# Kernel tuning notes

Measured on AMD Instinct MI355X. Metric: run time of the kernel, lower is better.

The kernel has to match this reference:

```python
import jax, jax.numpy as jnp
import numpy as np
import math

D_MODEL = 1024
D_STATE = 64
BATCH = 16
LENGTH = 4096


def _hippo_legs(n_dim: int) -> np.ndarray:
    """HiPPO-LegS matrix, scaled by 0.5 as in the torch module."""
    n = np.arange(n_dim)[:, None].astype(np.float32)
    k = np.arange(n_dim)[None, :].astype(np.float32)
    a = np.where(n > k, -np.sqrt(2.0 * n + 1.0) * np.sqrt(2.0 * k + 1.0), 0.0)
    a = a + np.diag(-(np.arange(n_dim, dtype=np.float32) + 1.0))
    return (a * 0.5).astype(np.float32)


def setup_inputs() -> dict:
    key = jax.random.key(0)
    k_u, k_B, k_C, k_dt = jax.random.split(key, 4)
    u = jax.random.normal(k_u, (BATCH, LENGTH, D_MODEL), dtype=jnp.float32)
    A = jnp.asarray(_hippo_legs(D_STATE))
    B = jax.random.normal(k_B, (D_STATE, D_MODEL), dtype=jnp.float32) * 0.01
    C = jax.random.normal(k_C, (D_MODEL, D_STATE), dtype=jnp.float32) * 0.01
    D = jnp.ones((D_MODEL,), dtype=jnp.float32)
    log_dt = (jax.random.uniform(k_dt, (D_MODEL,), dtype=jnp.float32)
              * (math.log(0.1) - math.log(0.001)) + math.log(0.001))
    return {"u": u, "A": A, "B": B, "C": C, "D": D, "log_dt": log_dt}


def reference(u, A, B, C, D, log_dt):
    # u: (B, L, d_model)
    d_state = A.shape[0]
    dt_mean = jnp.exp(log_dt).mean()
    a_bar = jnp.eye(d_state, dtype=u.dtype) + dt_mean * A  # (N, N)
    # Precompute input projection for every timestep: (L, B, N)
    bu = jnp.einsum('bld,nd->lbn', u, dt_mean * B)

    def step(x, bu_t):
        # x: (B, N); x_{t} = x_{t-1} @ a_bar.T + (u_t @ b_bar.T)
        x = x @ a_bar.T + bu_t
        return x, x

    x0 = jnp.zeros((u.shape[0], d_state), dtype=u.dtype)
    _, xs = jax.lax.scan(step, x0, bu)  # xs: (L, B, N)
    y = jnp.einsum('lbn,dn->bld', xs, C) + u * D  # (B, L, d_model)
    return y
```

## Files before the change

### kernel.cpp

```cpp
#include <hip/hip_runtime.h>


#define DM   1024
#define DS   64
#define NB   16
#define LL   4096
#define LC   64
#define NCH  (LL / LC)
#define MTOT (NB * LL)
#define NTASK (NB * NCH)

#define WS_ABAR 64
#define WS_APOW (WS_ABAR + 4096)
#define WS_TMP  (WS_APOW + 4096)
#define WS_E    (WS_TMP + 4096)
#define WS_S    (WS_E + NTASK * DS)
#define WS_BHI  143424
#define WS_CHI  (WS_BHI + 32768)
#define WS_XS   (WS_CHI + 32768)
#define WS_BU   (WS_XS + 2097152)

typedef __attribute__((ext_vector_type(4))) float f32x4;
typedef __attribute__((ext_vector_type(8))) short bf16x8;
typedef __attribute__((ext_vector_type(8))) unsigned short ushort8;

__device__ inline unsigned short bf16_rne(float f) {
    unsigned u = __builtin_bit_cast(unsigned, f);
    u += 0x7FFFu + ((u >> 16) & 1u);
    return (unsigned short)(u >> 16);
}

__global__ __launch_bounds__(256) void k_prep(const float* __restrict__ A,
                                              const float* __restrict__ log_dt,
                                              float* __restrict__ ws) {
    __shared__ float red[256];
    int tid = threadIdx.x;
    float s = 0.f;
    for (int i = tid; i < DM; i += 256) s += expf(log_dt[i]);
    red[tid] = s;
    __syncthreads();
    for (int off = 128; off > 0; off >>= 1) {
        if (tid < off) red[tid] += red[tid + off];
        __syncthreads();
    }
    float dt = red[0] * (1.f / (float)DM);
    if (tid == 0) ws[0] = dt;
    for (int idx = tid; idx < 4096; idx += 256) {
        int n = idx >> 6, m = idx & 63;
        ws[WS_ABAR + idx] = dt * A[idx] + ((n == m) ? 1.f : 0.f);
    }
}

__global__ __launch_bounds__(256) void k_cvt(const float* __restrict__ Bm,
                                             const float* __restrict__ C,
                                             float* __restrict__ ws) {
    int bid = blockIdx.x;
    int isC = bid >> 6;
    const float* src = isC ? C : Bm;
    unsigned short* dst = (unsigned short*)(ws + (isC ? WS_CHI : WS_BHI));
    float scale = isC ? 1.f : ws[0];
    int i = ((bid & 63) * 256 + threadIdx.x) * 4;
    float4 v = *reinterpret_cast<const float4*>(&src[i]);
    ushort4 h;
    h.x = bf16_rne(v.x * scale);
    h.y = bf16_rne(v.y * scale);
    h.z = bf16_rne(v.z * scale);
    h.w = bf16_rne(v.w * scale);
    *reinterpret_cast<ushort4*>(&dst[i]) = h;
}

__global__ __launch_bounds__(256) void k_matsq(const float* __restrict__ src,
                                               float* __restrict__ dst) {
    __shared__ float s[64][65];
    int tid = threadIdx.x;
#pragma unroll
    for (int rep = 0; rep < 16; ++rep) {
        int idx = rep * 256 + tid;
        s[idx >> 6][idx & 63] = src[idx];
    }
    __syncthreads();
    int n = (blockIdx.x << 2) + (tid >> 6);
    int m = tid & 63;
    float a0 = 0.f, a1 = 0.f, a2 = 0.f, a3 = 0.f;
#pragma unroll
    for (int k = 0; k < 64; k += 4) {
        a0 = fmaf(s[n][k + 0], s[k + 0][m], a0);
        a1 = fmaf(s[n][k + 1], s[k + 1][m], a1);
        a2 = fmaf(s[n][k + 2], s[k + 2][m], a2);
        a3 = fmaf(s[n][k + 3], s[k + 3][m], a3);
    }
    dst[(n << 6) + m] = (a0 + a1) + (a2 + a3);
}

__global__ __launch_bounds__(256, 4) void k_gemm1(const float* __restrict__ u,
                                                  const float* __restrict__ ws,
                                                  float* __restrict__ bu) {
    __shared__ short a_t[64][72];
    __shared__ short b_t[64][72];
    const unsigned short* bhig = (const unsigned short*)(ws + WS_BHI);
    int tid = threadIdx.x;
    int m0 = blockIdx.x * 64;
    int wid = tid >> 6, lane = tid & 63;
    int lr = lane & 15, lg = lane >> 4;
    int sr = tid >> 3, sc8 = (tid & 7) << 3;
    int bn = tid >> 3, bk8 = (tid & 7) << 3;

    f32x4 acc[4];
#pragma unroll
    for (int j = 0; j < 4; ++j) acc[j] = (f32x4)(0.f);

    float4 ra[2][2];
    ushort8 rb[2];
#pragma unroll
    for (int i = 0; i < 2; ++i) {
        ra[i][0] = *reinterpret_cast<const float4*>(&u[(size_t)(m0 + sr + 32 * i) * DM + sc8]);
        ra[i][1] = *reinterpret_cast<const float4*>(&u[(size_t)(m0 + sr + 32 * i) * DM + sc8 + 4]);
    }
#pragma unroll
    for (int j = 0; j < 2; ++j)
        rb[j] = *reinterpret_cast<const ushort8*>(&bhig[(size_t)(bn + 32 * j) * DM + bk8]);

    for (int kt = 0; kt < 16; ++kt) {
#pragma unroll
        for (int i = 0; i < 2; ++i) {
            ushort8 h;
            h[0] = bf16_rne(ra[i][0].x); h[1] = bf16_rne(ra[i][0].y);
            h[2] = bf16_rne(ra[i][0].z); h[3] = bf16_rne(ra[i][0].w);
            h[4] = bf16_rne(ra[i][1].x); h[5] = bf16_rne(ra[i][1].y);
            h[6] = bf16_rne(ra[i][1].z); h[7] = bf16_rne(ra[i][1].w);
            *reinterpret_cast<ushort8*>(&a_t[sr + 32 * i][sc8]) = h;
        }
#pragma unroll
        for (int j = 0; j < 2; ++j)
            *reinterpret_cast<ushort8*>(&b_t[bn + 32 * j][bk8]) = rb[j];
        __syncthreads();
        if (kt + 1 < 16) {
            int k0n = (kt + 1) * 64;
#pragma unroll
            for (int i = 0; i < 2; ++i) {
                ra[i][0] = *reinterpret_cast<const float4*>(&u[(size_t)(m0 + sr + 32 * i) * DM + k0n + sc8]);
                ra[i][1] = *reinterpret_cast<const float4*>(&u[(size_t)(m0 + sr + 32 * i) * DM + k0n + sc8 + 4]);
            }
#pragma unroll
            for (int j = 0; j < 2; ++j)
                rb[j] = *reinterpret_cast<const ushort8*>(&bhig[(size_t)(bn + 32 * j) * DM + k0n + bk8]);
        }
#pragma unroll
        for (int kf = 0; kf < 2; ++kf) {
            int kb = kf * 32 + lg * 8;
            bf16x8 af = *reinterpret_cast<bf16x8*>(&a_t[wid * 16 + lr][kb]);
#pragma unroll
            for (int nf = 0; nf < 4; ++nf) {
                bf16x8 bf_ = *reinterpret_cast<bf16x8*>(&b_t[nf * 16 + lr][kb]);
                acc[nf] = __builtin_amdgcn_mfma_f32_16x16x32_bf16(af, bf_, acc[nf], 0, 0, 0);
            }
        }
        __syncthreads();
    }
#pragma unroll
    for (int nf = 0; nf < 4; ++nf)
#pragma unroll
        for (int q = 0; q < 4; ++q) {
            size_t row = (size_t)(m0 + wid * 16 + lg * 4 + q);
            bu[row * DS + nf * 16 + lr] = acc[nf][q];
        }
}

template <int PASS>
__global__ __launch_bounds__(256) void k_scan(float* __restrict__ ws) {
    const float* Abar = ws + WS_ABAR;
    float* bu = ws + WS_BU;
    unsigned short* xs = (unsigned short*)(ws + WS_XS);
    int tid = threadIdx.x;
    int w = tid >> 6, lane = tid & 63;
    int t0 = blockIdx.x * 4 + w;
    int t1 = t0 + 512;
    __shared__ float xbuf[4][2][64];

    float a_row[64];
#pragma unroll
    for (int mg = 0; mg < 16; ++mg) {
        float4 v = *reinterpret_cast<const float4*>(&Abar[lane * 64 + mg * 4]);
        a_row[mg * 4 + 0] = v.x; a_row[mg * 4 + 1] = v.y;
        a_row[mg * 4 + 2] = v.z; a_row[mg * 4 + 3] = v.w;
    }
    float x0, x1;
    if (PASS == 0) { x0 = 0.f; x1 = 0.f; }
    else {
        x0 = ws[WS_S + (size_t)t0 * DS + lane];
        x1 = ws[WS_S + (size_t)t1 * DS + lane];
    }
    size_t r0 = (size_t)(t0 >> 6) * LL + (size_t)(t0 & 63) * LC;
    size_t r1 = (size_t)(t1 >> 6) * LL + (size_t)(t1 & 63) * LC;
    float* bub0 = bu + r0 * DS;
    float* bub1 = bu + r1 * DS;
    unsigned short* xp0 = xs + r0 * DS;
    unsigned short* xp1 = xs + r1 * DS;
    float v0 = bub0[lane], v1 = bub1[lane];
    for (int t = 0; t < LC; ++t) {
        float n0 = 0.f, n1 = 0.f;
        if (t + 1 < LC) {
            n0 = bub0[(t + 1) * DS + lane];
            n1 = bub1[(t + 1) * DS + lane];
        }
        xbuf[w][0][lane] = x0;
        xbuf[w][1][lane] = x1;
        asm volatile("" ::: "memory");
        float p0[4], p1[4];
#pragma unroll
        for (int g = 0; g < 4; ++g) {
            float acc0 = (g == 0) ? v0 : 0.f;
            float acc1 = (g == 0) ? v1 : 0.f;
#pragma unroll
            for (int q = 0; q < 4; ++q) {
                float4 m0v = *reinterpret_cast<float4*>(&xbuf[w][0][g * 16 + q * 4]);
                float4 m1v = *reinterpret_cast<float4*>(&xbuf[w][1][g * 16 + q * 4]);
                float c0 = a_row[g * 16 + q * 4 + 0], c1 = a_row[g * 16 + q * 4 + 1];
                float c2 = a_row[g * 16 + q * 4 + 2], c3 = a_row[g * 16 + q * 4 + 3];
                acc0 = fmaf(c0, m0v.x, acc0); acc1 = fmaf(c0, m1v.x, acc1);
                acc0 = fmaf(c1, m0v.y, acc0); acc1 = fmaf(c1, m1v.y, acc1);
                acc0 = fmaf(c2, m0v.z, acc0); acc1 = fmaf(c2, m1v.z, acc1);
                acc0 = fmaf(c3, m0v.w, acc0); acc1 = fmaf(c3, m1v.w, acc1);
            }
            p0[g] = acc0; p1[g] = acc1;
        }
        asm volatile("" ::: "memory");
        x0 = (p0[0] + p0[1]) + (p0[2] + p0[3]);
        x1 = (p1[0] + p1[1]) + (p1[2] + p1[3]);
        if (PASS == 1) {
            xp0[t * DS + lane] = bf16_rne(x0);
            xp1[t * DS + lane] = bf16_rne(x1);
        }
        v0 = n0; v1 = n1;
    }
    if (PASS == 0) {
        ws[WS_E + (size_t)t0 * DS + lane] = x0;
        ws[WS_E + (size_t)t1 * DS + lane] = x1;
    }
}

__global__ __launch_bounds__(64) void k_combine(float* __restrict__ ws) {
    const float* Apow = ws + WS_APOW;
    int b = blockIdx.x;
    int lane = threadIdx.x;
    __shared__ float xbuf[64];
    __shared__ float e_lds[NCH][64];
    const float* Eb = ws + WS_E + (size_t)b * NCH * DS;
#pragma unroll
    for (int r = 0; r < 16; ++r) {
        int idx = r * 64 + lane;
        int jj = idx >> 4, c4 = (idx & 15) << 2;
        *reinterpret_cast<float4*>(&e_lds[jj][c4]) =
            *reinterpret_cast<const float4*>(&Eb[jj * DS + c4]);
    }
    float p_row[64];
#pragma unroll
    for (int mg = 0; mg < 16; ++mg) {
        float4 v = *reinterpret_cast<const float4*>(&Apow[lane * 64 + mg * 4]);
        p_row[mg * 4 + 0] = v.x; p_row[mg * 4 + 1] = v.y;
        p_row[mg * 4 + 2] = v.z; p_row[mg * 4 + 3] = v.w;
    }
    __syncthreads();
    float x = 0.f;
    for (int jj = 0; jj < NCH; ++jj) {
        size_t task = (size_t)b * NCH + jj;
        ws[WS_S + task * DS + lane] = x;
        float e = e_lds[jj][lane];
        xbuf[lane] = x;
        asm volatile("" ::: "memory");
        float part[4];
#pragma unroll
        for (int g = 0; g < 4; ++g) {
            float acc = (g == 0) ? e : 0.f;
#pragma unroll
            for (int q = 0; q < 4; ++q) {
                float4 xm = *reinterpret_cast<float4*>(&xbuf[g * 16 + q * 4]);
                acc = fmaf(p_row[g * 16 + q * 4 + 0], xm.x, acc);
                acc = fmaf(p_row[g * 16 + q * 4 + 1], xm.y, acc);
                acc = fmaf(p_row[g * 16 + q * 4 + 2], xm.z, acc);
                acc = fmaf(p_row[g * 16 + q * 4 + 3], xm.w, acc);
            }
            part[g] = acc;
        }
        asm volatile("" ::: "memory");
        x = (part[0] + part[1]) + (part[2] + part[3]);
    }
}

__global__ __launch_bounds__(256, 4) void k_gemm2(const float* __restrict__ u,
                                                  const float* __restrict__ Dv,
                                                  const float* __restrict__ ws,
                                                  float* __restrict__ y) {
    __shared__ __align__(16) char smem[2 * 128 * 72 * 2];
    short (*a_t)[72] = (short(*)[72])(smem);
    short (*c_t)[72] = (short(*)[72])(smem + 18432);
    float (*out_lds)[132] = (float(*)[132])(smem);

    const unsigned short* xsb = (const unsigned short*)(ws + WS_XS);
    const unsigned short* chig = (const unsigned short*)(ws + WS_CHI);
    int tid = threadIdx.x;
    int m0 = blockIdx.x * 128;
    int d0 = blockIdx.y * 128;
    int wid = tid >> 6, lane = tid & 63;
    int lr = lane & 15, lg = lane >> 4;

#pragma unroll
    for (int rep = 0; rep < 4; ++rep) {
        int idx = rep * 256 + tid;
        int r = idx >> 3, k8 = (idx & 7) << 3;
        *reinterpret_cast<ushort8*>(&a_t[r][k8]) =
            *reinterpret_cast<const ushort8*>(&xsb[(size_t)(m0 + r) * DS + k8]);
    }
#pragma unroll
    for (int rep = 0; rep < 4; ++rep) {
        int idx = rep * 256 + tid;
        int dl = idx >> 3, n8 = (idx & 7) << 3;
        *reinterpret_cast<ushort8*>(&c_t[dl][n8]) =
            *reinterpret_cast<const ushort8*>(&chig[(size_t)(d0 + dl) * DS + n8]);
    }
    __syncthreads();

    f32x4 acc[2][8];
#pragma unroll
    for (int i = 0; i < 2; ++i)
#pragma unroll
        for (int j = 0; j < 8; ++j) acc[i][j] = (f32x4)(0.f);

#pragma unroll
    for (int kf = 0; kf < 2; ++kf) {
        int kb = kf * 32 + lg * 8;
        bf16x8 ah0 = *reinterpret_cast<bf16x8*>(&a_t[wid * 32 + lr][kb]);
        bf16x8 ah1 = *reinterpret_cast<bf16x8*>(&a_t[wid * 32 + 16 + lr][kb]);
#pragma unroll
        for (int nf = 0; nf < 8; ++nf) {
            bf16x8 cb = *reinterpret_cast<bf16x8*>(&c_t[nf * 16 + lr][kb]);
            acc[0][nf] = __builtin_amdgcn_mfma_f32_16x16x32_bf16(ah0, cb, acc[0][nf], 0, 0, 0);
            acc[1][nf] = __builtin_amdgcn_mfma_f32_16x16x32_bf16(ah1, cb, acc[1][nf], 0, 0, 0);
        }
    }
    __syncthreads();

#pragma unroll
    for (int h = 0; h < 2; ++h) {
        if ((wid >> 1) == h) {
            int rbase = (wid & 1) * 32;
#pragma unroll
            for (int mf = 0; mf < 2; ++mf)
#pragma unroll
                for (int nf = 0; nf < 8; ++nf)
#pragma unroll
                    for (int q = 0; q < 4; ++q)
                        out_lds[rbase + mf * 16 + lg * 4 + q][nf * 16 + lr] = acc[mf][nf][q];
        }
        __syncthreads();
#pragma unroll
        for (int rep = 0; rep < 8; ++rep) {
            int idx = rep * 256 + tid;
            int r = idx >> 5, c4 = (idx & 31) << 2;
            float4 a = *reinterpret_cast<float4*>(&out_lds[r][c4]);
            size_t row = (size_t)(m0 + h * 64 + r);
            int c = d0 + c4;
            float4 uv = *reinterpret_cast<const float4*>(&u[row * DM + c]);
            float4 dv = *reinterpret_cast<const float4*>(&Dv[c]);
            float4 o;
            o.x = a.x + uv.x * dv.x;
            o.y = a.y + uv.y * dv.y;
            o.z = a.z + uv.z * dv.z;
            o.w = a.w + uv.w * dv.w;
            *reinterpret_cast<float4*>(&y[row * DM + c]) = o;
        }
        __syncthreads();
    }
}

extern "C" void kernel_launch(void* const* d_in, const int* in_sizes, int n_in,
                              void* d_out, int out_size, void* d_ws, size_t ws_size,
                              hipStream_t stream) {
    (void)in_sizes; (void)n_in; (void)out_size; (void)ws_size;
    const float* u      = (const float*)d_in[0];
    const float* A      = (const float*)d_in[1];
    const float* Bm     = (const float*)d_in[2];
    const float* C      = (const float*)d_in[3];
    const float* Dv     = (const float*)d_in[4];
    const float* log_dt = (const float*)d_in[5];
    float* y  = (float*)d_out;
    float* ws = (float*)d_ws;
    float* bu = ws + WS_BU;

    k_prep<<<dim3(1), dim3(256), 0, stream>>>(A, log_dt, ws);
    k_cvt<<<dim3(128), dim3(256), 0, stream>>>(Bm, C, ws);
    k_matsq<<<dim3(16), dim3(256), 0, stream>>>(ws + WS_ABAR, ws + WS_TMP);
    k_matsq<<<dim3(16), dim3(256), 0, stream>>>(ws + WS_TMP,  ws + WS_APOW);
    k_matsq<<<dim3(16), dim3(256), 0, stream>>>(ws + WS_APOW, ws + WS_TMP);
    k_matsq<<<dim3(16), dim3(256), 0, stream>>>(ws + WS_TMP,  ws + WS_APOW);
    k_matsq<<<dim3(16), dim3(256), 0, stream>>>(ws + WS_APOW, ws + WS_TMP);
    k_matsq<<<dim3(16), dim3(256), 0, stream>>>(ws + WS_TMP,  ws + WS_APOW);

    k_gemm1<<<dim3(MTOT / 64), dim3(256), 0, stream>>>(u, ws, bu);
    k_scan<0><<<dim3(NTASK / 8), dim3(256), 0, stream>>>(ws);
    k_combine<<<dim3(NB), dim3(64), 0, stream>>>(ws);
    k_scan<1><<<dim3(NTASK / 8), dim3(256), 0, stream>>>(ws);
    k_gemm2<<<dim3(MTOT / 128, DM / 128), dim3(256), 0, stream>>>(u, Dv, ws, y);
}
```

Baseline: 349.6 us.

## Scan two timesteps per iteration using A^2 to halve serial dependency chain

The chunked scan now advances the state two steps at a time via x_{t+2} = A^2 x_t + (A b_t + b_{t+1}), keeping A^2 rows in registers, so the dependent matvec chain per chunk is halved. Each wave handles one chunk instead of two, and twice as many blocks are launched. The input-projection matvec is off the critical path, and pass 1 recomputes odd states separately. In exchange the per-step FLOPs and register pressure (two 64-float rows) go up. A trailing __syncthreads in gemm2 is also dropped on the last half-iteration.

```diff
diff --git a/kernel.cpp b/kernel.cpp
--- a/kernel.cpp
+++ b/kernel.cpp
@@ -11,11 +11,12 @@
 #define NTASK (NB * NCH)
 
 #define WS_ABAR 64
-#define WS_APOW (WS_ABAR + 4096)
-#define WS_TMP  (WS_APOW + 4096)
-#define WS_E    (WS_TMP + 4096)
+#define WS_A2   4160
+#define WS_APOW 8256
+#define WS_TMP  12352
+#define WS_E    16448
 #define WS_S    (WS_E + NTASK * DS)
-#define WS_BHI  143424
+#define WS_BHI  (WS_S + NTASK * DS)
 #define WS_CHI  (WS_BHI + 32768)
 #define WS_XS   (WS_CHI + 32768)
 #define WS_BU   (WS_XS + 2097152)
@@ -169,74 +170,94 @@
 template <int PASS>
 __global__ __launch_bounds__(256) void k_scan(float* __restrict__ ws) {
     const float* Abar = ws + WS_ABAR;
+    const float* A2m  = ws + WS_A2;
     float* bu = ws + WS_BU;
     unsigned short* xs = (unsigned short*)(ws + WS_XS);
     int tid = threadIdx.x;
     int w = tid >> 6, lane = tid & 63;
-    int t0 = blockIdx.x * 4 + w;
-    int t1 = t0 + 512;
-    __shared__ float xbuf[4][2][64];
-
-    float a_row[64];
+    int task = blockIdx.x * 4 + w;
+    __shared__ float xbuf[4][64];
+    __shared__ float bbuf[4][2][64];
+
+    float a_row[64], a2_row[64];
 #pragma unroll
     for (int mg = 0; mg < 16; ++mg) {
         float4 v = *reinterpret_cast<const float4*>(&Abar[lane * 64 + mg * 4]);
         a_row[mg * 4 + 0] = v.x; a_row[mg * 4 + 1] = v.y;
         a_row[mg * 4 + 2] = v.z; a_row[mg * 4 + 3] = v.w;
-    }
-    float x0, x1;
-    if (PASS == 0) { x0 = 0.f; x1 = 0.f; }
-    else {
-        x0 = ws[WS_S + (size_t)t0 * DS + lane];
-        x1 = ws[WS_S + (size_t)t1 * DS + lane];
-    }
-    size_t r0 = (size_t)(t0 >> 6) * LL + (size_t)(t0 & 63) * LC;
-    size_t r1 = (size_t)(t1 >> 6) * LL + (size_t)(t1 & 63) * LC;
-    float* bub0 = bu + r0 * DS;
-    float* bub1 = bu + r1 * DS;
-    unsigned short* xp0 = xs + r0 * DS;
-    unsigned short* xp1 = xs + r1 * DS;
-    float v0 = bub0[lane], v1 = bub1[lane];
-    for (int t = 0; t < LC; ++t) {
-        float n0 = 0.f, n1 = 0.f;
-        if (t + 1 < LC) {
-            n0 = bub0[(t + 1) * DS + lane];
-            n1 = bub1[(t + 1) * DS + lane];
-        }
-        xbuf[w][0][lane] = x0;
-        xbuf[w][1][lane] = x1;
+        float4 v2 = *reinterpret_cast<const float4*>(&A2m[lane * 64 + mg * 4]);
+        a2_row[mg * 4 + 0] = v2.x; a2_row[mg * 4 + 1] = v2.y;
+        a2_row[mg * 4 + 2] = v2.z; a2_row[mg * 4 + 3] = v2.w;
+    }
+    float x;
+    if (PASS == 0) x = 0.f;
+    else           x = ws[WS_S + (size_t)task * DS + lane];
+
+    size_t r0 = (size_t)(task >> 6) * LL + (size_t)(task & 63) * LC;
+    float* bub = bu + r0 * DS;
+    unsigned short* xp = xs + r0 * DS;
+
+    float b0v = bub[lane];
+    float b1v = bub[DS + lane];
+    bbuf[w][0][lane] = b0v;
+    asm volatile("" ::: "memory");
+
+    for (int i = 0; i < 32; ++i) {
+        float nb0 = bub[(2 * i + 2) * DS + lane];
+        float nb1 = bub[(2 * i + 3) * DS + lane];
+        xbuf[w][lane] = x;
         asm volatile("" ::: "memory");
-        float p0[4], p1[4];
+        float* bb = &bbuf[w][i & 1][0];
+        float bp[4];
 #pragma unroll
         for (int g = 0; g < 4; ++g) {
-            float acc0 = (g == 0) ? v0 : 0.f;
-            float acc1 = (g == 0) ? v1 : 0.f;
+            float acc = 0.f;
 #pragma unroll
             for (int q = 0; q < 4; ++q) {
-                float4 m0v = *reinterpret_cast<float4*>(&xbuf[w][0][g * 16 + q * 4]);
-                float4 m1v = *reinterpret_cast<float4*>(&xbuf[w][1][g * 16 + q * 4]);
-                float c0 = a_row[g * 16 + q * 4 + 0], c1 = a_row[g * 16 + q * 4 + 1];
-                float c2 = a_row[g * 16 + q * 4 + 2], c3 = a_row[g * 16 + q * 4 + 3];
-                acc0 = fmaf(c0, m0v.x, acc0); acc1 = fmaf(c0, m1v.x, acc1);
-                acc0 = fmaf(c1, m0v.y, acc0); acc1 = fmaf(c1, m1v.y, acc1);
-                acc0 = fmaf(c2, m0v.z, acc0); acc1 = fmaf(c2, m1v.z, acc1);
-                acc0 = fmaf(c3, m0v.w, acc0); acc1 = fmaf(c3, m1v.w, acc1);
+                float4 bm = *reinterpret_cast<float4*>(&bb[g * 16 + q * 4]);
+                acc = fmaf(a_row[g * 16 + q * 4 + 0], bm.x, acc);
+                acc = fmaf(a_row[g * 16 + q * 4 + 1], bm.y, acc);
+                acc = fmaf(a_row[g * 16 + q * 4 + 2], bm.z, acc);
+                acc = fmaf(a_row[g * 16 + q * 4 + 3], bm.w, acc);
             }
-            p0[g] = acc0; p1[g] = acc1;
+            bp[g] = acc;
+        }
+        float bdot = ((bp[0] + bp[1]) + (bp[2] + bp[3])) + b1v;
+        float p2[4], p1d[4];
+#pragma unroll
+        for (int g = 0; g < 4; ++g) {
+            float acc2 = 0.f, acc1 = 0.f;
+#pragma unroll
+            for (int q = 0; q < 4; ++q) {
+                float4 xm = *reinterpret_cast<float4*>(&xbuf[w][g * 16 + q * 4]);
+                float c20 = a2_row[g * 16 + q * 4 + 0], c21 = a2_row[g * 16 + q * 4 + 1];
+                float c22 = a2_row[g * 16 + q * 4 + 2], c23 = a2_row[g * 16 + q * 4 + 3];
+                acc2 = fmaf(c20, xm.x, acc2);
+                acc2 = fmaf(c21, xm.y, acc2);
+                acc2 = fmaf(c22, xm.z, acc2);
+                acc2 = fmaf(c23, xm.w, acc2);
+                if (PASS == 1) {
+                    float c10 = a_row[g * 16 + q * 4 + 0], c11 = a_row[g * 16 + q * 4 + 1];
+                    float c12 = a_row[g * 16 + q * 4 + 2], c13 = a_row[g * 16 + q * 4 + 3];
+                    acc1 = fmaf(c10, xm.x, acc1);
+                    acc1 = fmaf(c11, xm.y, acc1);
+                    acc1 = fmaf(c12, xm.z, acc1);
+                    acc1 = fmaf(c13, xm.w, acc1);
+                }
+            }
+            p2[g] = acc2; p1d[g] = acc1;
+        }
+        float xe = ((p2[0] + p2[1]) + (p2[2] + p2[3])) + bdot;
+        if (PASS == 1) {
+            float xo = ((p1d[0] + p1d[1]) + (p1d[2] + p1d[3])) + b0v;
+            xp[(2 * i) * DS + lane] = bf16_rne(xo);
+            xp[(2 * i + 1) * DS + lane] = bf16_rne(xe);
         }
         asm volatile("" ::: "memory");
-        x0 = (p0[0] + p0[1]) + (p0[2] + p0[3]);
-        x1 = (p1[0] + p1[1]) + (p1[2] + p1[3]);
-        if (PASS == 1) {
-            xp0[t * DS + lane] = bf16_rne(x0);
-            xp1[t * DS + lane] = bf16_rne(x1);
-        }
-        v0 = n0; v1 = n1;
-    }
-    if (PASS == 0) {
-        ws[WS_E + (size_t)t0 * DS + lane] = x0;
-        ws[WS_E + (size_t)t1 * DS + lane] = x1;
-    }
+        bbuf[w][(i + 1) & 1][lane] = nb0;
+        b0v = nb0; b1v = nb1; x = xe;
+    }
+    if (PASS == 0) ws[WS_E + (size_t)task * DS + lane] = x;
 }
 
 __global__ __launch_bounds__(64) void k_combine(float* __restrict__ ws) {
@@ -369,7 +390,7 @@
             o.w = a.w + uv.w * dv.w;
             *reinterpret_cast<float4*>(&y[row * DM + c]) = o;
         }
-        __syncthreads();
+        if (h == 0) __syncthreads();
     }
 }
 
@@ -389,16 +410,16 @@
 
     k_prep<<<dim3(1), dim3(256), 0, stream>>>(A, log_dt, ws);
     k_cvt<<<dim3(128), dim3(256), 0, stream>>>(Bm, C, ws);
-    k_matsq<<<dim3(16), dim3(256), 0, stream>>>(ws + WS_ABAR, ws + WS_TMP);
-    k_matsq<<<dim3(16), dim3(256), 0, stream>>>(ws + WS_TMP,  ws + WS_APOW);
+    k_matsq<<<dim3(16), dim3(256), 0, stream>>>(ws + WS_ABAR, ws + WS_A2);
+    k_matsq<<<dim3(16), dim3(256), 0, stream>>>(ws + WS_A2,   ws + WS_APOW);
     k_matsq<<<dim3(16), dim3(256), 0, stream>>>(ws + WS_APOW, ws + WS_TMP);
     k_matsq<<<dim3(16), dim3(256), 0, stream>>>(ws + WS_TMP,  ws + WS_APOW);
     k_matsq<<<dim3(16), dim3(256), 0, stream>>>(ws + WS_APOW, ws + WS_TMP);
     k_matsq<<<dim3(16), dim3(256), 0, stream>>>(ws + WS_TMP,  ws + WS_APOW);
 
     k_gemm1<<<dim3(MTOT / 64), dim3(256), 0, stream>>>(u, ws, bu);
-    k_scan<0><<<dim3(NTASK / 8), dim3(256), 0, stream>>>(ws);
+    k_scan<0><<<dim3(NTASK / 4), dim3(256), 0, stream>>>(ws);
     k_combine<<<dim3(NB), dim3(64), 0, stream>>>(ws);
-    k_scan<1><<<dim3(NTASK / 8), dim3(256), 0, stream>>>(ws);
+    k_scan<1><<<dim3(NTASK / 4), dim3(256), 0, stream>>>(ws);
     k_gemm2<<<dim3(MTOT / 128, DM / 128), dim3(256), 0, stream>>>(u, Dv, ws, y);
 }
```

Measured after the change: 336.8 us. 1.04x faster.
